# Kernel tuning notes

Hardware: AMD Instinct MI355X
Metric: run time of the kernel (lower is better)

## Reference

```python
import jax, jax.numpy as jnp
import numpy as np

C = 343.0      # speed of sound (init kwarg c)
F = 16         # number of frequency channels (len(omega))
H = 128        # MLP hidden width
N = 131072     # collocation points


def _mlp(coords, W1, b1, W2, b2, W3, b3):
    # coords: [..., 3] -> [..., 2F] (first F = real part, last F = imag part)
    h = jnp.tanh(coords @ W1 + b1)
    h = jnp.tanh(h @ W2 + b2)
    return h @ W3 + b3


def setup_inputs() -> dict:
    key = jax.random.key(0)
    ks = jax.random.split(key, 4)
    inputs = jax.random.normal(ks[0], (N, 3), dtype=jnp.float32)
    # omega = 2*pi*f for f = 100..1600 Hz (matches init kwarg list)
    omega = 2.0 * jnp.pi * 100.0 * jnp.arange(1, F + 1, dtype=jnp.float32)
    s_in = 1.0 / np.sqrt(3.0)
    s_h = 1.0 / np.sqrt(float(H))
    W1 = jax.random.normal(ks[1], (3, H), dtype=jnp.float32) * s_in
    b1 = jnp.zeros((H,), dtype=jnp.float32)
    W2 = jax.random.normal(ks[2], (H, H), dtype=jnp.float32) * s_h
    b2 = jnp.zeros((H,), dtype=jnp.float32)
    W3 = jax.random.normal(ks[3], (H, 2 * F), dtype=jnp.float32) * s_h
    b3 = jnp.zeros((2 * F,), dtype=jnp.float32)
    return {"inputs": inputs, "omega": omega, "W1": W1, "b1": b1,
            "W2": W2, "b2": b2, "W3": W3, "b3": b3}


def reference(inputs, omega, W1, b1, W2, b2, W3, b3):
    # Pointwise network R^3 -> R^{2F} (real/imag stacked).
    f = lambda c3: _mlp(c3, W1, b1, W2, b2, W3, b3)

    # u: complex pressure per point per frequency, [N, F]
    out = _mlp(inputs, W1, b1, W2, b2, W3, b3)           # [N, 2F]
    u = out[:, :F] + 1j * out[:, F:]

    # Full spatial Hessian per point via forward-over-reverse AD (fused
    # replacement for the torch per-channel autograd.grad loop).
    hess = jax.vmap(jax.jacfwd(jax.jacrev(f)))(inputs)   # [N, 2F, 3, 3]
    lap_ri = jnp.einsum('nfii->nf', hess)                # diagonal trace = Laplacian
    lap = lap_ri[:, :F] + 1j * lap_ri[:, F:]             # [N, F] complex

    # PDE residual skips channel 0, exactly as the torch loop (i+1 indexing).
    k2 = (omega[1:] / C) ** 2                            # [F-1]
    residual = lap[:, 1:] + k2 * u[:, 1:]                # [N, F-1]

    # mean over channels then over batch == global mean of |residual|^2
    return jnp.mean(jnp.abs(residual) ** 2)
```

## Files before the change

kernel.cpp:

```cpp
#include <hip/hip_runtime.h>
#include <math.h>

#ifndef __has_builtin
#define __has_builtin(x) 0
#endif

#define NPTS   131072
#define FCH    16
#define CSND   343.0f
#define PB     16
#define BLOCK  256
#define GRID   512
#define NBLK   (NPTS / PB)

typedef _Float16 half8 __attribute__((ext_vector_type(8)));
typedef _Float16 h2 __attribute__((ext_vector_type(2)));
typedef float    f32x4 __attribute__((ext_vector_type(4)));

static __device__ __forceinline__ h2 ph2(float a, float b) {
#if __has_builtin(__builtin_amdgcn_cvt_pkrtz)
  return __builtin_bit_cast(h2, __builtin_amdgcn_cvt_pkrtz(a, b));
#else
  h2 v; v[0] = (_Float16)a; v[1] = (_Float16)b;
  return v;
#endif
}
static __device__ __forceinline__ unsigned bc(h2 v) {
  return __builtin_bit_cast(unsigned, v);
}

static __device__ __forceinline__ float mytanh(float x) {
#if __has_builtin(__builtin_amdgcn_exp2f)
  float e = __builtin_amdgcn_exp2f(2.885390082f * x);
#else
  float e = __expf(2.0f * x);
#endif
  return fmaf(-2.0f, __builtin_amdgcn_rcpf(e + 1.0f), 1.0f);
}


__global__ __launch_bounds__(BLOCK, 2) void helmholtz_kernel(
    const float* __restrict__ x,
    const float* __restrict__ omega,
    const float* __restrict__ W1,
    const float* __restrict__ b1,
    const float* __restrict__ W2,
    const float* __restrict__ b2,
    const float* __restrict__ W3,
    const float* __restrict__ b3,
    float* __restrict__ out)
{
  __shared__ unsigned s_A[2][80 * 64];
  __shared__ unsigned s_HG[2][16 * 128];

  const int tid  = threadIdx.x;
  const int w    = tid >> 6;
  const int l    = tid & 63;
  const int col  = l & 15;
  const int quad = l >> 4;
  const int nh   = w & 1;

  const int pA = tid >> 4;
  const int g  = tid & 15;
  h2 wx2[4], wy2[4], wz2[4], bB2[4], m2wq2[4];
#pragma unroll
  for (int u2 = 0; u2 < 4; u2++) {
    int u0 = 8 * g + 2 * u2, u1 = u0 + 1;
    float ax = W1[u0], ay = W1[128 + u0], az = W1[256 + u0];
    float bx = W1[u1], by = W1[128 + u1], bz = W1[256 + u1];
    wx2[u2] = ph2(ax, bx); wy2[u2] = ph2(ay, by); wz2[u2] = ph2(az, bz);
    bB2[u2] = ph2(b1[u0], b1[u1]);
    m2wq2[u2] = ph2(-2.0f * (ax * ax + ay * ay + az * az),
                    -2.0f * (bx * bx + by * by + bz * bz));
  }

  half8 w2f[2][4];
#pragma unroll
  for (int ntl = 0; ntl < 2; ntl++) {
    const int n = 32 * w + 16 * ntl + col;
#pragma unroll
    for (int ks = 0; ks < 4; ks++) {
      half8 f;
#pragma unroll
      for (int j8 = 0; j8 < 8; j8++)
        f[j8] = (_Float16)W2[(ks * 32 + (quad << 3) + j8) * 128 + n];
      w2f[ntl][ks] = f;
    }
  }
  half8 w3f[4];
#pragma unroll
  for (int ks = 0; ks < 4; ks++) {
    half8 f;
#pragma unroll
    for (int j8 = 0; j8 < 8; j8++) {
      int kap = ks * 32 + (quad << 3) + j8;
      int q   = kap >> 1;
      int j   = 32 * (q >> 4) + 16 * (kap & 1) + (q & 15);
      f[j8] = (_Float16)W3[j * 32 + 16 * nh + col];
    }
    w3f[ks] = f;
  }

  const float b2r0 = b2[32 * w + col];
  const float b2r1 = b2[32 * w + 16 + col];
  float k2v = 0.0f;
  if (col >= 1) {
    float om = omega[col] * (1.0f / CSND);
    k2v = om * om;
  }
  const float b3v = b3[16 * nh + col];
  const h2 one2 = {(_Float16)1.0f, (_Float16)1.0f};
  const h2 m2c  = {(_Float16)-2.0f, (_Float16)-2.0f};

  float wsum = 0.0f;

  auto phaseA = [&](int blk, int buf) {
    const float* xp = x + (size_t)(blk * PB + pA) * 3;
    float x0 = xp[0], x1 = xp[1], x2 = xp[2];
    h2 xh0 = ph2(x0, x0), xh1 = ph2(x1, x1), xh2 = ph2(x2, x2);
    h2 tp[4], sp[4];
#pragma unroll
    for (int u2 = 0; u2 < 4; u2++) {
      h2 z = xh0 * wx2[u2] + xh1 * wy2[u2] + xh2 * wz2[u2] + bB2[u2];
      float t0 = mytanh((float)z[0]);
      float t1 = mytanh((float)z[1]);
      tp[u2] = ph2(t0, t1);
      sp[u2] = one2 - tp[u2] * tp[u2];
    }
    unsigned* sA = s_A[buf];
    const int cbase = (g ^ pA) << 2;
    uint4 q;
    q = make_uint4(bc(tp[0]), bc(tp[1]), bc(tp[2]), bc(tp[3]));
    *(uint4*)&sA[(pA)      * 64 + cbase] = q;
    q = make_uint4(bc(sp[0]*wx2[0]), bc(sp[1]*wx2[1]), bc(sp[2]*wx2[2]), bc(sp[3]*wx2[3]));
    *(uint4*)&sA[(16 + pA) * 64 + cbase] = q;
    q = make_uint4(bc(sp[0]*wy2[0]), bc(sp[1]*wy2[1]), bc(sp[2]*wy2[2]), bc(sp[3]*wy2[3]));
    *(uint4*)&sA[(32 + pA) * 64 + cbase] = q;
    q = make_uint4(bc(sp[0]*wz2[0]), bc(sp[1]*wz2[1]), bc(sp[2]*wz2[2]), bc(sp[3]*wz2[3]));
    *(uint4*)&sA[(48 + pA) * 64 + cbase] = q;
    q = make_uint4(bc((tp[0]*sp[0])*m2wq2[0]), bc((tp[1]*sp[1])*m2wq2[1]),
                   bc((tp[2]*sp[2])*m2wq2[2]), bc((tp[3]*sp[3])*m2wq2[3]));
    *(uint4*)&sA[(64 + pA) * 64 + cbase] = q;
  };

  auto phaseDE = [&](int buf) {
    const unsigned* hgb = s_HG[buf];
    const int pbase = col * 128;
    f32x4 dy = (f32x4){0.0f, 0.0f, 0.0f, 0.0f};
    f32x4 dl = (f32x4){0.0f, 0.0f, 0.0f, 0.0f};
#pragma unroll
    for (int ks = 0; ks < 4; ks++) {
      int pos = ((((ks << 2) + quad) ^ col) << 2);
      half8 afy = *(const half8*)&hgb[pbase + pos];
      half8 afl = *(const half8*)&hgb[pbase + 64 + pos];
      dy = __builtin_amdgcn_mfma_f32_16x16x32_f16(afy, w3f[ks], dy, 0, 0, 0);
      dl = __builtin_amdgcn_mfma_f32_16x16x32_f16(afl, w3f[ks], dl, 0, 0, 0);
    }
    if (col >= 1) {
#pragma unroll
      for (int r = 0; r < 4; r++) {
        float yv  = dy[r] + b3v;
        float res = fmaf(k2v, yv, dl[r]);
        wsum += res * res;
      }
    }
  };

  phaseA(blockIdx.x, 0);
  __syncthreads();

  int parity = 0;
  for (int blk = blockIdx.x; blk < NBLK; blk += gridDim.x, parity ^= 1) {
    if (w < 2 && blk != (int)blockIdx.x) phaseDE(parity ^ 1);

    int nblk = blk + (int)gridDim.x;
    if (nblk < NBLK) phaseA(nblk, parity ^ 1);

    const unsigned* sA = s_A[parity];
    f32x4 acc[5][2];
#pragma unroll
    for (int v = 0; v < 5; v++)
#pragma unroll
      for (int ntl = 0; ntl < 2; ntl++)
        acc[v][ntl] = (f32x4){0.0f, 0.0f, 0.0f, 0.0f};

#pragma unroll
    for (int v = 0; v < 5; v++) {
      const int rb = (v * 16 + col) * 64;
#pragma unroll
      for (int ks = 0; ks < 4; ks++) {
        half8 af = *(const half8*)&sA[rb + ((((ks << 2) + quad) ^ col) << 2)];
        acc[v][0] = __builtin_amdgcn_mfma_f32_16x16x32_f16(af, w2f[0][ks], acc[v][0], 0, 0, 0);
        acc[v][1] = __builtin_amdgcn_mfma_f32_16x16x32_f16(af, w2f[1][ks], acc[v][1], 0, 0, 0);
      }
    }

    {
      unsigned* hg = s_HG[parity];
#pragma unroll
      for (int r = 0; r < 4; r++) {
        int p = (quad << 2) + r;
        float t0 = mytanh(acc[0][0][r] + b2r0);
        float t1 = mytanh(acc[0][1][r] + b2r1);
        h2 tp = ph2(t0, t1);
        h2 sp = one2 - tp * tp;
        h2 d0 = ph2(acc[1][0][r], acc[1][1][r]);
        h2 d1 = ph2(acc[2][0][r], acc[2][1][r]);
        h2 d2 = ph2(acc[3][0][r], acc[3][1][r]);
        h2 Ap = ph2(acc[4][0][r], acc[4][1][r]);
        h2 Bp = d0 * d0 + d1 * d1 + d2 * d2;
        h2 gg = sp * (Ap + m2c * (tp * Bp));
        int q   = 16 * w + col;
        int pos = (((q >> 2) ^ p) << 2) + (q & 3);
        hg[p * 128 + pos]      = bc(tp);
        hg[p * 128 + 64 + pos] = bc(gg);
      }
    }
    __syncthreads();
  }

  if (w < 2) phaseDE(parity ^ 1);

#pragma unroll
  for (int off = 32; off > 0; off >>= 1)
    wsum += __shfl_down(wsum, off, 64);
  if (l == 0)
    atomicAdd(out, wsum * (1.0f / ((float)NPTS * (float)(FCH - 1))));
}

extern "C" void kernel_launch(void* const* d_in, const int* in_sizes, int n_in,
                              void* d_out, int out_size, void* d_ws, size_t ws_size,
                              hipStream_t stream) {
  const float* x     = (const float*)d_in[0];
  const float* omega = (const float*)d_in[1];
  const float* W1    = (const float*)d_in[2];
  const float* b1    = (const float*)d_in[3];
  const float* W2    = (const float*)d_in[4];
  const float* b2    = (const float*)d_in[5];
  const float* W3    = (const float*)d_in[6];
  const float* b3    = (const float*)d_in[7];
  float* out = (float*)d_out;

  (void)hipMemsetAsync(out, 0, sizeof(float), stream);
  helmholtz_kernel<<<GRID, BLOCK, 0, stream>>>(x, omega, W1, b1, W2, b2, W3, b3, out);
}
```

Measured before the change: 121.1 us.

## Shrink block to two waves with wider per-wave N tiles and single A buffer

Halves the block to 128 threads and doubles the grid, so each wave covers 64 hidden columns and reuses each A fragment across four MFMAs instead of two. Layer-one results are computed into registers before the MFMA phase and written to a single shared A buffer after a second barrier, replacing the double-buffered A. The directional-derivative squares are summed in fp32 before packing. This frees LDS and improves fragment reuse, at the cost of an extra barrier per iteration and more live registers (w2f and accumulators doubled), which may limit occupancy.

```diff
diff --git a/kernel.cpp b/kernel.cpp
--- a/kernel.cpp
+++ b/kernel.cpp
@@ -9,8 +9,8 @@
 #define FCH    16
 #define CSND   343.0f
 #define PB     16
-#define BLOCK  256
-#define GRID   512
+#define BLOCK  128
+#define GRID   1024
 #define NBLK   (NPTS / PB)
 
 typedef _Float16 half8 __attribute__((ext_vector_type(8)));
@@ -50,22 +50,22 @@
     const float* __restrict__ b3,
     float* __restrict__ out)
 {
-  __shared__ unsigned s_A[2][80 * 64];
+  __shared__ unsigned s_A[80 * 64];
   __shared__ unsigned s_HG[2][16 * 128];
 
   const int tid  = threadIdx.x;
-  const int w    = tid >> 6;
+  const int wv   = tid >> 6;
   const int l    = tid & 63;
   const int col  = l & 15;
   const int quad = l >> 4;
-  const int nh   = w & 1;
-
-  const int pA = tid >> 4;
-  const int g  = tid & 15;
-  h2 wx2[4], wy2[4], wz2[4], bB2[4], m2wq2[4];
-#pragma unroll
-  for (int u2 = 0; u2 < 4; u2++) {
-    int u0 = 8 * g + 2 * u2, u1 = u0 + 1;
+  const int nh   = wv;
+
+  const int pA = tid >> 3;
+  const int g8 = tid & 7;
+  h2 wx2[8], wy2[8], wz2[8], bB2[8], m2wq2[8];
+#pragma unroll
+  for (int u2 = 0; u2 < 8; u2++) {
+    int u0 = 16 * g8 + 2 * u2, u1 = u0 + 1;
     float ax = W1[u0], ay = W1[128 + u0], az = W1[256 + u0];
     float bx = W1[u1], by = W1[128 + u1], bz = W1[256 + u1];
     wx2[u2] = ph2(ax, bx); wy2[u2] = ph2(ay, by); wz2[u2] = ph2(az, bz);
@@ -74,17 +74,17 @@
                     -2.0f * (bx * bx + by * by + bz * bz));
   }
 
-  half8 w2f[2][4];
-#pragma unroll
-  for (int ntl = 0; ntl < 2; ntl++) {
-    const int n = 32 * w + 16 * ntl + col;
+  half8 w2f[4][4];
+#pragma unroll
+  for (int t4 = 0; t4 < 4; t4++) {
+    const int n = 64 * wv + 16 * t4 + col;
 #pragma unroll
     for (int ks = 0; ks < 4; ks++) {
       half8 f;
 #pragma unroll
       for (int j8 = 0; j8 < 8; j8++)
         f[j8] = (_Float16)W2[(ks * 32 + (quad << 3) + j8) * 128 + n];
-      w2f[ntl][ks] = f;
+      w2f[t4][ks] = f;
     }
   }
   half8 w3f[4];
@@ -101,8 +101,9 @@
     w3f[ks] = f;
   }
 
-  const float b2r0 = b2[32 * w + col];
-  const float b2r1 = b2[32 * w + 16 + col];
+  float b2r[4];
+#pragma unroll
+  for (int t4 = 0; t4 < 4; t4++) b2r[t4] = b2[64 * wv + 16 * t4 + col];
   float k2v = 0.0f;
   if (col >= 1) {
     float om = omega[col] * (1.0f / CSND);
@@ -113,34 +114,40 @@
   const h2 m2c  = {(_Float16)-2.0f, (_Float16)-2.0f};
 
   float wsum = 0.0f;
-
-  auto phaseA = [&](int blk, int buf) {
+  h2 tp8[8], sp8[8];
+
+  auto computeA = [&](int blk) {
     const float* xp = x + (size_t)(blk * PB + pA) * 3;
     float x0 = xp[0], x1 = xp[1], x2 = xp[2];
     h2 xh0 = ph2(x0, x0), xh1 = ph2(x1, x1), xh2 = ph2(x2, x2);
-    h2 tp[4], sp[4];
-#pragma unroll
-    for (int u2 = 0; u2 < 4; u2++) {
+#pragma unroll
+    for (int u2 = 0; u2 < 8; u2++) {
       h2 z = xh0 * wx2[u2] + xh1 * wy2[u2] + xh2 * wz2[u2] + bB2[u2];
-      float t0 = mytanh((float)z[0]);
-      float t1 = mytanh((float)z[1]);
-      tp[u2] = ph2(t0, t1);
-      sp[u2] = one2 - tp[u2] * tp[u2];
-    }
-    unsigned* sA = s_A[buf];
-    const int cbase = (g ^ pA) << 2;
-    uint4 q;
-    q = make_uint4(bc(tp[0]), bc(tp[1]), bc(tp[2]), bc(tp[3]));
-    *(uint4*)&sA[(pA)      * 64 + cbase] = q;
-    q = make_uint4(bc(sp[0]*wx2[0]), bc(sp[1]*wx2[1]), bc(sp[2]*wx2[2]), bc(sp[3]*wx2[3]));
-    *(uint4*)&sA[(16 + pA) * 64 + cbase] = q;
-    q = make_uint4(bc(sp[0]*wy2[0]), bc(sp[1]*wy2[1]), bc(sp[2]*wy2[2]), bc(sp[3]*wy2[3]));
-    *(uint4*)&sA[(32 + pA) * 64 + cbase] = q;
-    q = make_uint4(bc(sp[0]*wz2[0]), bc(sp[1]*wz2[1]), bc(sp[2]*wz2[2]), bc(sp[3]*wz2[3]));
-    *(uint4*)&sA[(48 + pA) * 64 + cbase] = q;
-    q = make_uint4(bc((tp[0]*sp[0])*m2wq2[0]), bc((tp[1]*sp[1])*m2wq2[1]),
-                   bc((tp[2]*sp[2])*m2wq2[2]), bc((tp[3]*sp[3])*m2wq2[3]));
-    *(uint4*)&sA[(64 + pA) * 64 + cbase] = q;
+      tp8[u2] = ph2(mytanh((float)z[0]), mytanh((float)z[1]));
+      sp8[u2] = one2 - tp8[u2] * tp8[u2];
+    }
+  };
+  auto storeA = [&]() {
+    const int c0 = ((2 * g8)     ^ pA) << 2;
+    const int c1 = ((2 * g8 + 1) ^ pA) << 2;
+    uint4 qa, qb;
+    qa = make_uint4(bc(tp8[0]), bc(tp8[1]), bc(tp8[2]), bc(tp8[3]));
+    qb = make_uint4(bc(tp8[4]), bc(tp8[5]), bc(tp8[6]), bc(tp8[7]));
+    *(uint4*)&s_A[pA * 64 + c0] = qa;  *(uint4*)&s_A[pA * 64 + c1] = qb;
+    qa = make_uint4(bc(sp8[0]*wx2[0]), bc(sp8[1]*wx2[1]), bc(sp8[2]*wx2[2]), bc(sp8[3]*wx2[3]));
+    qb = make_uint4(bc(sp8[4]*wx2[4]), bc(sp8[5]*wx2[5]), bc(sp8[6]*wx2[6]), bc(sp8[7]*wx2[7]));
+    *(uint4*)&s_A[(16 + pA) * 64 + c0] = qa;  *(uint4*)&s_A[(16 + pA) * 64 + c1] = qb;
+    qa = make_uint4(bc(sp8[0]*wy2[0]), bc(sp8[1]*wy2[1]), bc(sp8[2]*wy2[2]), bc(sp8[3]*wy2[3]));
+    qb = make_uint4(bc(sp8[4]*wy2[4]), bc(sp8[5]*wy2[5]), bc(sp8[6]*wy2[6]), bc(sp8[7]*wy2[7]));
+    *(uint4*)&s_A[(32 + pA) * 64 + c0] = qa;  *(uint4*)&s_A[(32 + pA) * 64 + c1] = qb;
+    qa = make_uint4(bc(sp8[0]*wz2[0]), bc(sp8[1]*wz2[1]), bc(sp8[2]*wz2[2]), bc(sp8[3]*wz2[3]));
+    qb = make_uint4(bc(sp8[4]*wz2[4]), bc(sp8[5]*wz2[5]), bc(sp8[6]*wz2[6]), bc(sp8[7]*wz2[7]));
+    *(uint4*)&s_A[(48 + pA) * 64 + c0] = qa;  *(uint4*)&s_A[(48 + pA) * 64 + c1] = qb;
+    qa = make_uint4(bc((tp8[0]*sp8[0])*m2wq2[0]), bc((tp8[1]*sp8[1])*m2wq2[1]),
+                    bc((tp8[2]*sp8[2])*m2wq2[2]), bc((tp8[3]*sp8[3])*m2wq2[3]));
+    qb = make_uint4(bc((tp8[4]*sp8[4])*m2wq2[4]), bc((tp8[5]*sp8[5])*m2wq2[5]),
+                    bc((tp8[6]*sp8[6])*m2wq2[6]), bc((tp8[7]*sp8[7])*m2wq2[7]));
+    *(uint4*)&s_A[(64 + pA) * 64 + c0] = qa;  *(uint4*)&s_A[(64 + pA) * 64 + c1] = qb;
   };
 
   auto phaseDE = [&](int buf) {
@@ -166,32 +173,66 @@
     }
   };
 
-  phaseA(blockIdx.x, 0);
+  computeA(blockIdx.x);
+  storeA();
   __syncthreads();
 
   int parity = 0;
-  for (int blk = blockIdx.x; blk < NBLK; blk += gridDim.x, parity ^= 1) {
-    if (w < 2 && blk != (int)blockIdx.x) phaseDE(parity ^ 1);
+  bool first = true;
+  for (int blk = blockIdx.x; blk < NBLK; blk += gridDim.x) {
+    if (!first) phaseDE(parity ^ 1);
+    first = false;
 
     int nblk = blk + (int)gridDim.x;
-    if (nblk < NBLK) phaseA(nblk, parity ^ 1);
-
-    const unsigned* sA = s_A[parity];
-    f32x4 acc[5][2];
-#pragma unroll
-    for (int v = 0; v < 5; v++)
-#pragma unroll
-      for (int ntl = 0; ntl < 2; ntl++)
-        acc[v][ntl] = (f32x4){0.0f, 0.0f, 0.0f, 0.0f};
-
-#pragma unroll
-    for (int v = 0; v < 5; v++) {
-      const int rb = (v * 16 + col) * 64;
+    bool hasNext = (nblk < NBLK);
+    if (hasNext) computeA(nblk);
+
+    f32x4 bsum[4], acch[4], accc[4];
+    {
+      f32x4 accd[3][4];
+#pragma unroll
+      for (int d = 0; d < 3; d++)
+#pragma unroll
+        for (int t4 = 0; t4 < 4; t4++)
+          accd[d][t4] = (f32x4){0.0f, 0.0f, 0.0f, 0.0f};
+#pragma unroll
+      for (int d = 0; d < 3; d++) {
+        const int rb = ((d + 1) * 16 + col) * 64;
+#pragma unroll
+        for (int ks = 0; ks < 4; ks++) {
+          half8 af = *(const half8*)&s_A[rb + ((((ks << 2) + quad) ^ col) << 2)];
+          accd[d][0] = __builtin_amdgcn_mfma_f32_16x16x32_f16(af, w2f[0][ks], accd[d][0], 0, 0, 0);
+          accd[d][1] = __builtin_amdgcn_mfma_f32_16x16x32_f16(af, w2f[1][ks], accd[d][1], 0, 0, 0);
+          accd[d][2] = __builtin_amdgcn_mfma_f32_16x16x32_f16(af, w2f[2][ks], accd[d][2], 0, 0, 0);
+          accd[d][3] = __builtin_amdgcn_mfma_f32_16x16x32_f16(af, w2f[3][ks], accd[d][3], 0, 0, 0);
+        }
+      }
+#pragma unroll
+      for (int t4 = 0; t4 < 4; t4++)
+        bsum[t4] = accd[0][t4] * accd[0][t4] + accd[1][t4] * accd[1][t4]
+                 + accd[2][t4] * accd[2][t4];
+    }
+    {
+#pragma unroll
+      for (int t4 = 0; t4 < 4; t4++) {
+        acch[t4] = (f32x4){0.0f, 0.0f, 0.0f, 0.0f};
+        accc[t4] = (f32x4){0.0f, 0.0f, 0.0f, 0.0f};
+      }
+      const int rb0 = (col) * 64;
+      const int rb4 = (64 + col) * 64;
 #pragma unroll
       for (int ks = 0; ks < 4; ks++) {
-        half8 af = *(const half8*)&sA[rb + ((((ks << 2) + quad) ^ col) << 2)];
-        acc[v][0] = __builtin_amdgcn_mfma_f32_16x16x32_f16(af, w2f[0][ks], acc[v][0], 0, 0, 0);
-        acc[v][1] = __builtin_amdgcn_mfma_f32_16x16x32_f16(af, w2f[1][ks], acc[v][1], 0, 0, 0);
+        int pos = ((((ks << 2) + quad) ^ col) << 2);
+        half8 afh = *(const half8*)&s_A[rb0 + pos];
+        half8 afc = *(const half8*)&s_A[rb4 + pos];
+        acch[0] = __builtin_amdgcn_mfma_f32_16x16x32_f16(afh, w2f[0][ks], acch[0], 0, 0, 0);
+        acch[1] = __builtin_amdgcn_mfma_f32_16x16x32_f16(afh, w2f[1][ks], acch[1], 0, 0, 0);
+        acch[2] = __builtin_amdgcn_mfma_f32_16x16x32_f16(afh, w2f[2][ks], acch[2], 0, 0, 0);
+        acch[3] = __builtin_amdgcn_mfma_f32_16x16x32_f16(afh, w2f[3][ks], acch[3], 0, 0, 0);
+        accc[0] = __builtin_amdgcn_mfma_f32_16x16x32_f16(afc, w2f[0][ks], accc[0], 0, 0, 0);
+        accc[1] = __builtin_amdgcn_mfma_f32_16x16x32_f16(afc, w2f[1][ks], accc[1], 0, 0, 0);
+        accc[2] = __builtin_amdgcn_mfma_f32_16x16x32_f16(afc, w2f[2][ks], accc[2], 0, 0, 0);
+        accc[3] = __builtin_amdgcn_mfma_f32_16x16x32_f16(afc, w2f[3][ks], accc[3], 0, 0, 0);
       }
     }
 
@@ -200,26 +241,33 @@
 #pragma unroll
       for (int r = 0; r < 4; r++) {
         int p = (quad << 2) + r;
-        float t0 = mytanh(acc[0][0][r] + b2r0);
-        float t1 = mytanh(acc[0][1][r] + b2r1);
-        h2 tp = ph2(t0, t1);
-        h2 sp = one2 - tp * tp;
-        h2 d0 = ph2(acc[1][0][r], acc[1][1][r]);
-        h2 d1 = ph2(acc[2][0][r], acc[2][1][r]);
-        h2 d2 = ph2(acc[3][0][r], acc[3][1][r]);
-        h2 Ap = ph2(acc[4][0][r], acc[4][1][r]);
-        h2 Bp = d0 * d0 + d1 * d1 + d2 * d2;
-        h2 gg = sp * (Ap + m2c * (tp * Bp));
-        int q   = 16 * w + col;
-        int pos = (((q >> 2) ^ p) << 2) + (q & 3);
-        hg[p * 128 + pos]      = bc(tp);
-        hg[p * 128 + 64 + pos] = bc(gg);
+        float t2s[4];
+#pragma unroll
+        for (int t4 = 0; t4 < 4; t4++)
+          t2s[t4] = mytanh(acch[t4][r] + b2r[t4]);
+#pragma unroll
+        for (int tp_ = 0; tp_ < 2; tp_++) {
+          h2 tpk = ph2(t2s[2 * tp_], t2s[2 * tp_ + 1]);
+          h2 spk = one2 - tpk * tpk;
+          h2 Apk = ph2(accc[2 * tp_][r], accc[2 * tp_ + 1][r]);
+          h2 Bpk = ph2(bsum[2 * tp_][r], bsum[2 * tp_ + 1][r]);
+          h2 ggk = spk * (Apk + m2c * (tpk * Bpk));
+          int q   = 16 * (2 * wv + tp_) + col;
+          int pos = (((q >> 2) ^ p) << 2) + (q & 3);
+          hg[p * 128 + pos]      = bc(tpk);
+          hg[p * 128 + 64 + pos] = bc(ggk);
+        }
       }
     }
     __syncthreads();
-  }
-
-  if (w < 2) phaseDE(parity ^ 1);
+
+    if (hasNext) storeA();
+    __syncthreads();
+
+    parity ^= 1;
+  }
+
+  phaseDE(parity ^ 1);
 
 #pragma unroll
   for (int off = 32; off > 0; off >>= 1)
```

Result: slower. 127.7 us (+5.4%).
